# Kernel tuning notes

Measured on AMD Instinct MI355X. Metric: run time of the kernel, lower is better.

Reference implementation:

```python
import jax, jax.numpy as jnp
import numpy as np

B, T, D = 32, 576, 1024          # T = (384//16)**2 patches
H, G, HD = 16, 4, 64             # num_heads, query_groups, head_dim
BASE = 10000.0
SCALE = 1.0 / float(np.sqrt(HD))


def _rope2d(x):
    # x: [B, T, nH, HD]; 2D rotary: split head_dim into 4 groups of freq_dim.
    b, t, nh, hd = x.shape
    fd = hd // 4
    grid = int(np.sqrt(t))
    inv_freq = 1.0 / (BASE ** (jnp.arange(fd, dtype=jnp.float32) / fd))  # [fd]
    pos = jnp.arange(grid, dtype=jnp.float32)
    gx, gy = jnp.meshgrid(pos, pos, indexing='ij')          # [grid, grid]
    theta_x = gx.reshape(-1)[:, None] * inv_freq            # [T, fd]
    theta_y = gy.reshape(-1)[:, None] * inv_freq            # [T, fd]
    sx = jnp.sin(theta_x)[None, :, None, :]                 # [1, T, 1, fd]
    cx = jnp.cos(theta_x)[None, :, None, :]
    sy = jnp.sin(theta_y)[None, :, None, :]
    cy = jnp.cos(theta_y)[None, :, None, :]
    xr = x.reshape(b, t, nh, 4, fd)
    x1, x2, y1, y2 = xr[..., 0, :], xr[..., 1, :], xr[..., 2, :], xr[..., 3, :]
    out = jnp.stack([x1 * cx - x2 * sx,
                     x1 * sx + x2 * cx,
                     y1 * cy - y2 * sy,
                     y1 * sy + y2 * cy], axis=-2)           # [B, T, nH, 4, fd]
    return out.reshape(b, t, nh, hd)


def setup_inputs() -> dict:
    key = jax.random.key(0)
    k1, k2, k3 = jax.random.split(key, 3)
    x = jax.random.normal(k1, (B, T, D), dtype=jnp.float32)
    w_qkv = jax.random.normal(k2, (H * HD + 2 * G * HD, D), dtype=jnp.float32) * 0.02
    w_o = jax.random.normal(k3, (D, H * HD), dtype=jnp.float32) * 0.02
    return {"x": x, "w_qkv": w_qkv, "w_o": w_o, "window_size": -1}


def reference(x, w_qkv, w_o, window_size):
    # window_size=-1 -> full (non-windowed) attention, matching SDPA fallback.
    b, t, _ = x.shape
    qkv = x @ w_qkv.T                                       # [B, T, H*HD + 2*G*HD]
    q, k, v = jnp.split(qkv, [H * HD, H * HD + G * HD], axis=-1)
    q = q.reshape(b, t, H, HD)
    k = k.reshape(b, t, G, HD)
    v = v.reshape(b, t, G, HD)
    q = _rope2d(q)
    k = _rope2d(k)
    q = q.transpose(0, 2, 1, 3)                             # [B, H, T, HD]
    k = k.transpose(0, 2, 1, 3)                             # [B, G, T, HD]
    v = v.transpose(0, 2, 1, 3)
    hpg = H // G
    k = jnp.repeat(k, hpg, axis=1)                          # [B, H, T, HD]
    v = jnp.repeat(v, hpg, axis=1)
    scores = jnp.einsum('bhqd,bhkd->bhqk', q, k) * SCALE    # [B, H, T, T]
    attn = jax.nn.softmax(scores, axis=-1)
    out = jnp.einsum('bhqk,bhkd->bhqd', attn, v)            # [B, H, T, HD]
    out = out.transpose(0, 2, 1, 3).reshape(b, t, H * HD)
    return out @ w_o.T                                      # [B, T, D]
```

## Files before the change

kernel.cpp:

```cpp
#include <hip/hip_runtime.h>

typedef unsigned short u16;
typedef unsigned long long u64;
typedef __attribute__((ext_vector_type(8))) short short8;
typedef __attribute__((ext_vector_type(4))) float f32x4;

#define B_ 32
#define T_ 576
#define H_ 16
#define G_ 4
#define HD_ 64
#define DM 1024
#define NQKV 1536
#define BT (B_*T_)
#define GRID2D 24
#define FD 16

__device__ __forceinline__ u16 f2bf(float f) {
  unsigned u = __float_as_uint(f);
  u = (u + 0x7FFFu + ((u >> 16) & 1u)) >> 16;
  return (u16)u;
}
__device__ __forceinline__ float exp2v(float x) {
  float r;
  asm("v_exp_f32 %0, %1" : "=v"(r) : "v"(x));
  return r;
}

__device__ __forceinline__ void gl_lds16(const u16* g, u16* lds) {
  __builtin_amdgcn_global_load_lds((const __attribute__((address_space(1))) unsigned int*)g,
                                   (__attribute__((address_space(3))) unsigned int*)lds, 16, 0, 0);
}

#define WAITBAR(N)                                        \
  __builtin_amdgcn_sched_barrier(0);                      \
  asm volatile("s_waitcnt vmcnt(" #N ")\n\ts_barrier" ::: "memory"); \
  __builtin_amdgcn_sched_barrier(0);

__device__ __forceinline__ void cvt4(const float4* __restrict__ in, u16* __restrict__ o, int i) {
  float4 v = in[i];
  u64 pk = (u64)f2bf(v.x) | ((u64)f2bf(v.y) << 16) | ((u64)f2bf(v.z) << 32) | ((u64)f2bf(v.w) << 48);
  *(u64*)(o + (size_t)i * 4) = pk;
}

#define NX4 (BT*DM/4)
#define NQ4 (NQKV*DM/4)
#define NW4 (DM*DM/4)

__global__ __launch_bounds__(256) void prep_kernel(const float4* __restrict__ x, const float4* __restrict__ wq,
                                                   const float4* __restrict__ wo,
                                                   u16* __restrict__ xb, u16* __restrict__ wqb,
                                                   u16* __restrict__ wob, float4* __restrict__ tab) {
  int i = blockIdx.x * 256 + threadIdx.x;
  if (i < NX4) { cvt4(x, xb, i); return; }
  i -= NX4;
  if (i < NQ4) { cvt4(wq, wqb, i); return; }
  i -= NQ4;
  if (i < NW4) { cvt4(wo, wob, i); return; }
  i -= NW4;
  if (i >= T_ * FD) return;
  int t = i >> 4, j = i & 15;
  float inv = powf(10000.0f, -(float)j / 16.0f);
  float tx = (float)(t / GRID2D) * inv;
  float ty = (float)(t % GRID2D) * inv;
  float4 r;
  r.x = sinf(tx); r.y = cosf(tx); r.z = sinf(ty); r.w = cosf(ty);
  tab[i] = r;
}

__device__ __forceinline__ void stage_ab(const u16* __restrict__ A, const u16* __restrict__ Bw,
                                         int m0, int n0, int k0, u16* Asb, u16* Bsb,
                                         int w, int srow, int skk) {
#pragma unroll
  for (int ii = 0; ii < 2; ++ii) {
    int i = w * 2 + ii;
    int row = i * 16 + srow;
    gl_lds16(A + (size_t)(m0 + row) * DM + k0 + skk, Asb + i * 512);
    gl_lds16(Bw + (size_t)(n0 + row) * DM + k0 + skk, Bsb + i * 512);
  }
}

template <int EPI, int NX>
__global__ __launch_bounds__(256) void gemm_nt(const u16* __restrict__ A, const u16* __restrict__ Bw,
                                               u16* __restrict__ o0, u16* __restrict__ o1,
                                               u16* __restrict__ o2, float* __restrict__ fo,
                                               const float4* __restrict__ tab) {
  __shared__ __align__(16) u16 SMEM[24576];
  u16* const Asb = SMEM;
  u16* const Bsb = SMEM + 12288;
  const int tid = threadIdx.x;
  const int w = tid >> 6, l = tid & 63;
  const int wm = w >> 1, wn = w & 1;
  const int L = blockIdx.y * NX + blockIdx.x;
  const int cpx = (NX * 144) / 8;
  const int W = (L & 7) * cpx + (L >> 3);
  const int by = W / NX, bx = W - by * NX;
  const int m0 = by * 128, n0 = bx * 128;
  const int lr = l & 15, lg = l >> 4;
  const int srow = l >> 2;
  const int skk = (l & 3) * 8;
  f32x4 acc[4][4] = {};

#define COMPUTE(buf)                                                                        \
  {                                                                                         \
    short8 af[4], bfr[4];                                                                   \
    _Pragma("unroll") for (int mi = 0; mi < 4; ++mi)                                        \
        af[mi] = *(const short8*)(&Asb[(buf) * 4096 + (wm * 64 + mi * 16 + lr) * 32 + lg * 8]);  \
    _Pragma("unroll") for (int ni = 0; ni < 4; ++ni)                                        \
        bfr[ni] = *(const short8*)(&Bsb[(buf) * 4096 + (wn * 64 + ni * 16 + lr) * 32 + lg * 8]); \
    __builtin_amdgcn_s_setprio(1);                                                          \
    _Pragma("unroll") for (int mi = 0; mi < 4; ++mi)                                        \
        _Pragma("unroll") for (int ni = 0; ni < 4; ++ni)                                    \
            acc[mi][ni] = __builtin_amdgcn_mfma_f32_16x16x32_bf16(af[mi], bfr[ni],          \
                                                                  acc[mi][ni], 0, 0, 0);    \
    __builtin_amdgcn_s_setprio(0);                                                          \
  }

  stage_ab(A, Bw, m0, n0, 0,  Asb, Bsb, w, srow, skk);
  stage_ab(A, Bw, m0, n0, 32, Asb + 4096, Bsb + 4096, w, srow, skk);
  WAITBAR(4)

  int ic = 0;
  for (int t = 0; t < 30; ++t) {
    int in2 = ic + 2; if (in2 >= 3) in2 -= 3;
    stage_ab(A, Bw, m0, n0, (t + 2) * 32, Asb + in2 * 4096, Bsb + in2 * 4096, w, srow, skk);
    COMPUTE(ic);
    WAITBAR(4)
    ++ic; if (ic == 3) ic = 0;
  }
  COMPUTE(0);
  WAITBAR(0)
  COMPUTE(1);
#undef COMPUTE

  if (EPI == 0) {
    const float qs = 0.125f * 1.44269504f;
    const int nbase = n0 + wn * 64;
    if (nbase >= 1280) {
      const int g = (nbase - 1280) >> 6;
      const int brow = m0 + wm * 64;
      const int bb = brow / T_, t0 = brow - bb * T_;
      u16* tb = SMEM + w * 5120;
      __syncthreads();
#pragma unroll
      for (int mi = 0; mi < 4; ++mi)
#pragma unroll
        for (int ni = 0; ni < 4; ++ni) {
          u64 pk = (u64)f2bf(acc[mi][ni][0]) | ((u64)f2bf(acc[mi][ni][1]) << 16) |
                   ((u64)f2bf(acc[mi][ni][2]) << 32) | ((u64)f2bf(acc[mi][ni][3]) << 48);
          *(u64*)(tb + (ni * 16 + lr) * 80 + mi * 16 + lg * 4) = pk;
        }
      __syncthreads();
      u16* dst = o2 + ((size_t)(bb * G_ + g) * 64 + l) * T_ + t0;
      const u16* src = tb + l * 80;
#pragma unroll
      for (int j = 0; j < 8; ++j)
        *(short8*)(dst + j * 8) = *(const short8*)(src + j * 8);
    } else {
#pragma unroll
      for (int mi = 0; mi < 4; ++mi) {
#pragma unroll
        for (int r = 0; r < 4; ++r) {
          int mg = m0 + wm * 64 + mi * 16 + lg * 4 + r;
          int bb = mg / T_, t = mg - bb * T_;
          float v0 = acc[mi][0][r], v1 = acc[mi][1][r], v2 = acc[mi][2][r], v3 = acc[mi][3][r];
          float4 tb = tab[t * FD + lr];
          float sc = (nbase < 1024) ? qs : 1.0f;
          float e0 = (v0 * tb.y - v1 * tb.x) * sc;
          float e1 = (v0 * tb.x + v1 * tb.y) * sc;
          float e2 = (v2 * tb.w - v3 * tb.z) * sc;
          float e3 = (v2 * tb.z + v3 * tb.w) * sc;
          u16* dst;
          if (nbase < 1024) {
            int h = nbase >> 6;
            dst = o0 + (((size_t)bb * H_ + h) * T_ + t) * 64 + lr;
          } else {
            int g = (nbase - 1024) >> 6;
            dst = o1 + (((size_t)bb * G_ + g) * T_ + t) * 64 + lr;
          }
          dst[0] = f2bf(e0); dst[16] = f2bf(e1); dst[32] = f2bf(e2); dst[48] = f2bf(e3);
        }
      }
    }
  } else {
#pragma unroll
    for (int mi = 0; mi < 4; ++mi)
#pragma unroll
      for (int ni = 0; ni < 4; ++ni)
#pragma unroll
        for (int r = 0; r < 4; ++r) {
          int mg = m0 + wm * 64 + mi * 16 + lg * 4 + r;
          int ng = n0 + wn * 64 + ni * 16 + lr;
          fo[(size_t)mg * 1024 + ng] = acc[mi][ni][r];
        }
  }
}

__device__ __forceinline__ void stage_kv(const u16* __restrict__ k, const u16* __restrict__ vt,
                                         size_t kvbase, int kt, u16* Ksb, u16* Vsb,
                                         int w, int srow, int sblk) {
#pragma unroll
  for (int ii = 0; ii < 2; ++ii) {
    int i = w * 2 + ii;
    int row = i * 8 + srow;
    gl_lds16(k + kvbase + (size_t)(kt * 64 + row) * 64 + sblk * 8, Ksb + i * 512);
    gl_lds16(vt + kvbase + (size_t)row * T_ + kt * 64 + sblk * 8, Vsb + i * 512);
  }
}

__global__ __launch_bounds__(256) void attn_kernel(const u16* __restrict__ q, const u16* __restrict__ k,
                                                   const u16* __restrict__ vt, u16* __restrict__ o) {
  __shared__ __align__(16) u16 Ks[2][64 * 64];
  __shared__ __align__(16) u16 Vs[2][64 * 64];
  __shared__ __align__(16) u16 Pl[4][16 * 64];
  int L = blockIdx.x;
  int W = (L & 7) * 576 + (L >> 3);
  int qt = W % 9;
  int bh = W / 9;
  int h = bh & 15, b = bh >> 4;
  int g = h >> 2;
  int tid = threadIdx.x;
  int w = tid >> 6, l = tid & 63;
  int lr = l & 15, lg = l >> 4;
  const size_t kvbase = ((size_t)(b * G_ + g)) * (T_ * 64);

  const u16* qptr = q + (((size_t)(b * H_ + h)) * T_ + qt * 64 + w * 16 + lr) * 64;
  short8 qf0 = *(const short8*)(qptr + lg * 8);
  short8 qf1 = *(const short8*)(qptr + 32 + lg * 8);

  float ls[4] = {0.f, 0.f, 0.f, 0.f};
  f32x4 oacc[4];
#pragma unroll
  for (int dt = 0; dt < 4; ++dt) oacc[dt] = (f32x4){0.f, 0.f, 0.f, 0.f};

  const int srow = l >> 3;
  const int sblk = (l & 7) ^ (srow & 7);

  stage_kv(k, vt, kvbase, 0, &Ks[0][0], &Vs[0][0], w, srow, sblk);
  WAITBAR(0)

  int cur = 0;
  for (int kt = 0; kt < 9; ++kt) {
    if (kt < 8)
      stage_kv(k, vt, kvbase, kt + 1, &Ks[cur ^ 1][0], &Vs[cur ^ 1][0], w, srow, sblk);

    f32x4 sacc[4];
#pragma unroll
    for (int ct = 0; ct < 4; ++ct) {
      sacc[ct] = (f32x4){0.f, 0.f, 0.f, 0.f};
      int row = ct * 16 + lr;
      int i0 = (0 * 4 + lg) ^ (row & 7);
      int i1 = (1 * 4 + lg) ^ (row & 7);
      short8 kf0 = *(const short8*)(&Ks[cur][row * 64 + i0 * 8]);
      short8 kf1 = *(const short8*)(&Ks[cur][row * 64 + i1 * 8]);
      sacc[ct] = __builtin_amdgcn_mfma_f32_16x16x32_bf16(qf0, kf0, sacc[ct], 0, 0, 0);
      sacc[ct] = __builtin_amdgcn_mfma_f32_16x16x32_bf16(qf1, kf1, sacc[ct], 0, 0, 0);
    }

    float p[4][4];
#pragma unroll
    for (int ct = 0; ct < 4; ++ct)
#pragma unroll
      for (int r = 0; r < 4; ++r) p[ct][r] = exp2v(sacc[ct][r]);
#pragma unroll
    for (int r = 0; r < 4; ++r) ls[r] += (p[0][r] + p[1][r]) + (p[2][r] + p[3][r]);

    u16* pl = &Pl[w][0];
#pragma unroll
    for (int ct = 0; ct < 4; ++ct)
#pragma unroll
      for (int r = 0; r < 4; ++r) {
        int prow = lg * 4 + r;
        int pblk = (ct * 2 + (lr >> 3)) ^ (prow & 7);
        pl[prow * 64 + pblk * 8 + (lr & 7)] = (u16)((__float_as_uint(p[ct][r]) + 0x8000u) >> 16);
      }
    __builtin_amdgcn_sched_barrier(0);
    asm volatile("s_waitcnt lgkmcnt(0)" ::: "memory");
    __builtin_amdgcn_sched_barrier(0);
#pragma unroll
    for (int c = 0; c < 2; ++c) {
      int rblk = (c * 4 + lg) ^ (lr & 7);
      short8 pf = *(const short8*)(pl + lr * 64 + rblk * 8);
#pragma unroll
      for (int dt = 0; dt < 4; ++dt) {
        int row = dt * 16 + lr;
        int blk = (c * 4 + lg) ^ (row & 7);
        short8 vf = *(const short8*)(&Vs[cur][row * 64 + blk * 8]);
        oacc[dt] = __builtin_amdgcn_mfma_f32_16x16x32_bf16(pf, vf, oacc[dt], 0, 0, 0);
      }
    }

    if (kt < 8) {
      WAITBAR(0)
      cur ^= 1;
    }
  }

#pragma unroll
  for (int mk = 1; mk <= 8; mk <<= 1)
#pragma unroll
    for (int r = 0; r < 4; ++r) ls[r] += __shfl_xor(ls[r], mk);

#pragma unroll
  for (int dt = 0; dt < 4; ++dt)
#pragma unroll
    for (int r = 0; r < 4; ++r) {
      int trow = qt * 64 + w * 16 + lg * 4 + r;
      float v = oacc[dt][r] / ls[r];
      o[((size_t)b * T_ + trow) * 1024 + h * 64 + dt * 16 + lr] = f2bf(v);
    }
}

extern "C" void kernel_launch(void* const* d_in, const int* in_sizes, int n_in,
                              void* d_out, int out_size, void* d_ws, size_t ws_size,
                              hipStream_t stream) {
  const float* x = (const float*)d_in[0];
  const float* wqkv = (const float*)d_in[1];
  const float* wo = (const float*)d_in[2];
  float* out = (float*)d_out;

  u16* ws = (u16*)d_ws;
  u16* xb = ws;
  u16* wqkvb = xb + (size_t)BT * DM;
  u16* wob = wqkvb + (size_t)NQKV * DM;
  u16* qb = wob + (size_t)DM * DM;
  u16* kb = qb + (size_t)BT * DM;
  u16* vtb = kb + (size_t)B_ * G_ * T_ * 64;
  float4* tab = (float4*)(vtb + (size_t)B_ * G_ * T_ * 64);
  u16* ob = xb;

  const int prep_items = NX4 + NQ4 + NW4 + T_ * FD;
  prep_kernel<<<(prep_items + 255) / 256, 256, 0, stream>>>(
      (const float4*)x, (const float4*)wqkv, (const float4*)wo, xb, wqkvb, wob, tab);
  gemm_nt<0, 12><<<dim3(12, 144), 256, 0, stream>>>(xb, wqkvb, qb, kb, vtb, nullptr, tab);
  attn_kernel<<<B_ * H_ * 9, 256, 0, stream>>>(qb, kb, vtb, ob);
  gemm_nt<1, 8><<<dim3(8, 144), 256, 0, stream>>>(ob, wob, nullptr, nullptr, nullptr, out, nullptr);
}
```

Baseline: 251.6 us.

## Process two query tiles per attention block to reuse staged K/V

Each attention block now handles 128 query rows (two 64-row tiles) instead of 64, so every staged K/V tile in LDS is reused by two sets of MFMAs. The grid shrinks from 9 to 5 query tiles per (batch, head), which halves K/V global loads and LDS staging per query row. The fifth tile has only 64 valid rows, so its B half computes redundant work that is discarded at store time. Register pressure and P scratch LDS both roughly double, which may reduce occupancy.

```diff
diff --git a/kernel.cpp b/kernel.cpp
--- a/kernel.cpp
+++ b/kernel.cpp
@@ -212,11 +212,11 @@
                                                    const u16* __restrict__ vt, u16* __restrict__ o) {
   __shared__ __align__(16) u16 Ks[2][64 * 64];
   __shared__ __align__(16) u16 Vs[2][64 * 64];
-  __shared__ __align__(16) u16 Pl[4][16 * 64];
+  __shared__ __align__(16) u16 Pl[4][2][16 * 64];
   int L = blockIdx.x;
-  int W = (L & 7) * 576 + (L >> 3);
-  int qt = W % 9;
-  int bh = W / 9;
+  int W = (L & 7) * 320 + (L >> 3);
+  int qt = W % 5;
+  int bh = W / 5;
   int h = bh & 15, b = bh >> 4;
   int g = h >> 2;
   int tid = threadIdx.x;
@@ -224,14 +224,23 @@
   int lr = l & 15, lg = l >> 4;
   const size_t kvbase = ((size_t)(b * G_ + g)) * (T_ * 64);
 
-  const u16* qptr = q + (((size_t)(b * H_ + h)) * T_ + qt * 64 + w * 16 + lr) * 64;
-  short8 qf0 = *(const short8*)(qptr + lg * 8);
-  short8 qf1 = *(const short8*)(qptr + 32 + lg * 8);
-
-  float ls[4] = {0.f, 0.f, 0.f, 0.f};
-  f32x4 oacc[4];
-#pragma unroll
-  for (int dt = 0; dt < 4; ++dt) oacc[dt] = (f32x4){0.f, 0.f, 0.f, 0.f};
+  const bool okB = (qt < 4);
+  const int qrA = qt * 128 + w * 16;
+  const int qrB = okB ? (qrA + 64) : qrA;
+  const u16* qpA = q + (((size_t)(b * H_ + h)) * T_ + qrA + lr) * 64;
+  const u16* qpB = q + (((size_t)(b * H_ + h)) * T_ + qrB + lr) * 64;
+  short8 qfA0 = *(const short8*)(qpA + lg * 8);
+  short8 qfA1 = *(const short8*)(qpA + 32 + lg * 8);
+  short8 qfB0 = *(const short8*)(qpB + lg * 8);
+  short8 qfB1 = *(const short8*)(qpB + 32 + lg * 8);
+
+  float lsA[4] = {0.f, 0.f, 0.f, 0.f}, lsB[4] = {0.f, 0.f, 0.f, 0.f};
+  f32x4 oaccA[4], oaccB[4];
+#pragma unroll
+  for (int dt = 0; dt < 4; ++dt) {
+    oaccA[dt] = (f32x4){0.f, 0.f, 0.f, 0.f};
+    oaccB[dt] = (f32x4){0.f, 0.f, 0.f, 0.f};
+  }
 
   const int srow = l >> 3;
   const int sblk = (l & 7) ^ (srow & 7);
@@ -244,49 +253,56 @@
     if (kt < 8)
       stage_kv(k, vt, kvbase, kt + 1, &Ks[cur ^ 1][0], &Vs[cur ^ 1][0], w, srow, sblk);
 
-    f32x4 sacc[4];
+    f32x4 sA[4], sB[4];
 #pragma unroll
     for (int ct = 0; ct < 4; ++ct) {
-      sacc[ct] = (f32x4){0.f, 0.f, 0.f, 0.f};
+      sA[ct] = (f32x4){0.f, 0.f, 0.f, 0.f};
+      sB[ct] = (f32x4){0.f, 0.f, 0.f, 0.f};
       int row = ct * 16 + lr;
       int i0 = (0 * 4 + lg) ^ (row & 7);
       int i1 = (1 * 4 + lg) ^ (row & 7);
       short8 kf0 = *(const short8*)(&Ks[cur][row * 64 + i0 * 8]);
       short8 kf1 = *(const short8*)(&Ks[cur][row * 64 + i1 * 8]);
-      sacc[ct] = __builtin_amdgcn_mfma_f32_16x16x32_bf16(qf0, kf0, sacc[ct], 0, 0, 0);
-      sacc[ct] = __builtin_amdgcn_mfma_f32_16x16x32_bf16(qf1, kf1, sacc[ct], 0, 0, 0);
-    }
-
-    float p[4][4];
-#pragma unroll
-    for (int ct = 0; ct < 4; ++ct)
-#pragma unroll
-      for (int r = 0; r < 4; ++r) p[ct][r] = exp2v(sacc[ct][r]);
-#pragma unroll
-    for (int r = 0; r < 4; ++r) ls[r] += (p[0][r] + p[1][r]) + (p[2][r] + p[3][r]);
-
-    u16* pl = &Pl[w][0];
-#pragma unroll
-    for (int ct = 0; ct < 4; ++ct)
+      sA[ct] = __builtin_amdgcn_mfma_f32_16x16x32_bf16(qfA0, kf0, sA[ct], 0, 0, 0);
+      sA[ct] = __builtin_amdgcn_mfma_f32_16x16x32_bf16(qfA1, kf1, sA[ct], 0, 0, 0);
+      sB[ct] = __builtin_amdgcn_mfma_f32_16x16x32_bf16(qfB0, kf0, sB[ct], 0, 0, 0);
+      sB[ct] = __builtin_amdgcn_mfma_f32_16x16x32_bf16(qfB1, kf1, sB[ct], 0, 0, 0);
+    }
+
+    u16* plA = &Pl[w][0][0];
+    u16* plB = &Pl[w][1][0];
+#pragma unroll
+    for (int ct = 0; ct < 4; ++ct) {
+      float pA[4], pB[4];
+#pragma unroll
+      for (int r = 0; r < 4; ++r) { pA[r] = exp2v(sA[ct][r]); pB[r] = exp2v(sB[ct][r]); }
+#pragma unroll
+      for (int r = 0; r < 4; ++r) { lsA[r] += pA[r]; lsB[r] += pB[r]; }
 #pragma unroll
       for (int r = 0; r < 4; ++r) {
         int prow = lg * 4 + r;
         int pblk = (ct * 2 + (lr >> 3)) ^ (prow & 7);
-        pl[prow * 64 + pblk * 8 + (lr & 7)] = (u16)((__float_as_uint(p[ct][r]) + 0x8000u) >> 16);
+        int off = prow * 64 + pblk * 8 + (lr & 7);
+        plA[off] = (u16)((__float_as_uint(pA[r]) + 0x8000u) >> 16);
+        plB[off] = (u16)((__float_as_uint(pB[r]) + 0x8000u) >> 16);
       }
+    }
     __builtin_amdgcn_sched_barrier(0);
     asm volatile("s_waitcnt lgkmcnt(0)" ::: "memory");
     __builtin_amdgcn_sched_barrier(0);
+
 #pragma unroll
     for (int c = 0; c < 2; ++c) {
       int rblk = (c * 4 + lg) ^ (lr & 7);
-      short8 pf = *(const short8*)(pl + lr * 64 + rblk * 8);
+      short8 pfA = *(const short8*)(plA + lr * 64 + rblk * 8);
+      short8 pfB = *(const short8*)(plB + lr * 64 + rblk * 8);
 #pragma unroll
       for (int dt = 0; dt < 4; ++dt) {
         int row = dt * 16 + lr;
         int blk = (c * 4 + lg) ^ (row & 7);
         short8 vf = *(const short8*)(&Vs[cur][row * 64 + blk * 8]);
-        oacc[dt] = __builtin_amdgcn_mfma_f32_16x16x32_bf16(pf, vf, oacc[dt], 0, 0, 0);
+        oaccA[dt] = __builtin_amdgcn_mfma_f32_16x16x32_bf16(pfA, vf, oaccA[dt], 0, 0, 0);
+        oaccB[dt] = __builtin_amdgcn_mfma_f32_16x16x32_bf16(pfB, vf, oaccB[dt], 0, 0, 0);
       }
     }
 
@@ -299,16 +315,26 @@
 #pragma unroll
   for (int mk = 1; mk <= 8; mk <<= 1)
 #pragma unroll
-    for (int r = 0; r < 4; ++r) ls[r] += __shfl_xor(ls[r], mk);
+    for (int r = 0; r < 4; ++r) { lsA[r] += __shfl_xor(lsA[r], mk); lsB[r] += __shfl_xor(lsB[r], mk); }
 
 #pragma unroll
   for (int dt = 0; dt < 4; ++dt)
 #pragma unroll
     for (int r = 0; r < 4; ++r) {
-      int trow = qt * 64 + w * 16 + lg * 4 + r;
-      float v = oacc[dt][r] / ls[r];
-      o[((size_t)b * T_ + trow) * 1024 + h * 64 + dt * 16 + lr] = f2bf(v);
-    }
+      int trowA = qt * 128 + w * 16 + lg * 4 + r;
+      float vA = oaccA[dt][r] / lsA[r];
+      o[((size_t)b * T_ + trowA) * 1024 + h * 64 + dt * 16 + lr] = f2bf(vA);
+    }
+  if (okB) {
+#pragma unroll
+    for (int dt = 0; dt < 4; ++dt)
+#pragma unroll
+      for (int r = 0; r < 4; ++r) {
+        int trowB = qt * 128 + 64 + w * 16 + lg * 4 + r;
+        float vB = oaccB[dt][r] / lsB[r];
+        o[((size_t)b * T_ + trowB) * 1024 + h * 64 + dt * 16 + lr] = f2bf(vB);
+      }
+  }
 }
 
 extern "C" void kernel_launch(void* const* d_in, const int* in_sizes, int n_in,
@@ -333,6 +359,6 @@
   prep_kernel<<<(prep_items + 255) / 256, 256, 0, stream>>>(
       (const float4*)x, (const float4*)wqkv, (const float4*)wo, xb, wqkvb, wob, tab);
   gemm_nt<0, 12><<<dim3(12, 144), 256, 0, stream>>>(xb, wqkvb, qb, kb, vtb, nullptr, tab);
-  attn_kernel<<<B_ * H_ * 9, 256, 0, stream>>>(qb, kb, vtb, ob);
+  attn_kernel<<<B_ * H_ * 5, 256, 0, stream>>>(qb, kb, vtb, ob);
   gemm_nt<1, 8><<<dim3(8, 144), 256, 0, stream>>>(ob, wob, nullptr, nullptr, nullptr, out, nullptr);
 }
```

New measurement: 243.1 us (median of 2 runs). -3.4%, faster.
